# Kernel tuning notes

Measured on AMD Instinct MI355X. Metric: run time of the kernel, lower is better.

The kernel has to match this reference:

```python
import jax, jax.numpy as jnp
import numpy as np

N_NODES = 50000
N_EDGES = 800000
IN_DIM = 128
OUT_DIM = 64
REL_DIM = 32
NEG_SLOPE = 0.01  # torch F.leaky_relu default


def setup_inputs() -> dict:
    key = jax.random.key(0)
    k1, k2, k3, k4, k5, k6 = jax.random.split(key, 6)
    h = jax.random.normal(k1, (N_NODES, IN_DIM), dtype=jnp.float32)
    p = jax.random.normal(k2, (N_EDGES, REL_DIM), dtype=jnp.float32)
    src = jax.random.randint(k3, (N_EDGES,), 0, N_NODES, dtype=jnp.int32)
    dst = jax.random.randint(k4, (N_EDGES,), 0, N_NODES, dtype=jnp.int32)
    # torch Linear weights: [out_features, in_features], xavier-like scale
    W_fc = jax.random.normal(k5, (OUT_DIM, IN_DIM), dtype=jnp.float32) * (2.0 / (IN_DIM + OUT_DIM)) ** 0.5
    W_attn = jax.random.normal(k6, (1, 2 * OUT_DIM + REL_DIM), dtype=jnp.float32) * 0.1
    return {"h": h, "p": p, "src": src, "dst": dst, "W_fc": W_fc, "W_attn": W_attn}


def reference(h, p, src, dst, W_fc, W_attn):
    n = h.shape[0]
    z = h @ W_fc.T                       # [N, out_dim]
    z_src = z[src]                       # [E, out_dim] gather
    z_dst = z[dst]                       # [E, out_dim] gather
    feat = jnp.concatenate([z_src, p, z_dst], axis=1)  # [E, 2*out+rel]
    a = feat @ W_attn.T                  # [E, 1]
    e = jax.nn.leaky_relu(a[:, 0], NEG_SLOPE)          # [E]
    # segment softmax over incoming edges of each dst node
    seg_max = jax.ops.segment_max(e, dst, num_segments=n)  # [N]
    num = jnp.exp(e - seg_max[dst])                        # [E]
    denom = jax.ops.segment_sum(num, dst, num_segments=n)  # [N]
    alpha = num / denom[dst]                               # [E]
    # softmax-weighted message aggregation (scatter-add)
    h_out = jax.ops.segment_sum(alpha[:, None] * z_src, dst, num_segments=n)  # [N, out_dim]
    return h_out
```

## Files before the change

### kernel.cpp

```cpp
#include <hip/hip_runtime.h>
#include <hip/hip_bf16.h>

#define N_NODES 50000
#define N_EDGES 800000
#define IN_DIM 128
#define OUT_DIM 64
#define REL_DIM 32
#define NEG_SLOPE 0.01f
#define NB 391
#define K3_TILE 2048
#define K3_BLOCKS ((N_EDGES + K3_TILE - 1) / K3_TILE)
#define BWIN 2560
#define NBLK_A 782
#define K12_GRID 2346

__global__ __launch_bounds__(256) void k12_fused(const float* __restrict__ h,
                                                 const float* __restrict__ Wfc,
                                                 const float* __restrict__ Wattn,
                                                 const float* __restrict__ p,
                                                 __hip_bfloat16* __restrict__ zb,
                                                 float* __restrict__ s1,
                                                 float* __restrict__ s2,
                                                 float* __restrict__ dotp,
                                                 unsigned* __restrict__ ccur) {
    __shared__ float Wl[64][68];
    __shared__ float hl[64][68];
    const int t = threadIdx.x;
    const int b = blockIdx.x;

    if (b % 3 == 0) {
        const int blk = b / 3;
        const int cg = t & 15, ng = t >> 4;
        const int c0 = cg * 4;
        float wa1[4], wa2[4];
#pragma unroll
        for (int j = 0; j < 4; ++j) { wa1[j] = Wattn[c0 + j]; wa2[j] = Wattn[96 + c0 + j]; }

        const int n0 = blk * 64;
        float acc[4][4] = {};
        const float4* W4 = (const float4*)Wfc;
        const float4* h4 = (const float4*)h;

#pragma unroll
        for (int H = 0; H < 2; ++H) {
            __syncthreads();
#pragma unroll
            for (int i = 0; i < 4; ++i) {
                int idx = t + 256 * i;
                int c = idx & 63, k4 = idx >> 6;
                float4 v = W4[c * 32 + H * 16 + k4];
                Wl[4*k4+0][c] = v.x; Wl[4*k4+1][c] = v.y;
                Wl[4*k4+2][c] = v.z; Wl[4*k4+3][c] = v.w;
            }
#pragma unroll
            for (int i = 0; i < 4; ++i) {
                int idx = t + 256 * i;
                int n = idx & 63, k4 = idx >> 6;
                int gn = n0 + n; if (gn > N_NODES - 1) gn = N_NODES - 1;
                float4 v = h4[(size_t)gn * 32 + H * 16 + k4];
                hl[4*k4+0][n] = v.x; hl[4*k4+1][n] = v.y;
                hl[4*k4+2][n] = v.z; hl[4*k4+3][n] = v.w;
            }
            __syncthreads();
#pragma unroll 8
            for (int k = 0; k < 64; ++k) {
                float4 wv = *(const float4*)&Wl[k][c0];
                float4 hv = *(const float4*)&hl[k][ng * 4];
                float wvf[4] = {wv.x, wv.y, wv.z, wv.w};
                float hvf[4] = {hv.x, hv.y, hv.z, hv.w};
#pragma unroll
                for (int i = 0; i < 4; ++i)
#pragma unroll
                    for (int j = 0; j < 4; ++j) acc[i][j] += hvf[i] * wvf[j];
            }
        }

#pragma unroll
        for (int i = 0; i < 4; ++i) {
            int gn = n0 + ng * 4 + i;
            float r1 = acc[i][0]*wa1[0] + acc[i][1]*wa1[1] + acc[i][2]*wa1[2] + acc[i][3]*wa1[3];
            float r2 = acc[i][0]*wa2[0] + acc[i][1]*wa2[1] + acc[i][2]*wa2[2] + acc[i][3]*wa2[3];
#pragma unroll
            for (int off = 1; off < 16; off <<= 1) {
                r1 += __shfl_xor(r1, off, 64);
                r2 += __shfl_xor(r2, off, 64);
            }
            if (gn < N_NODES) {
                __hip_bfloat16 b0 = __float2bfloat16(acc[i][0]);
                __hip_bfloat16 b1 = __float2bfloat16(acc[i][1]);
                __hip_bfloat16 b2 = __float2bfloat16(acc[i][2]);
                __hip_bfloat16 b3 = __float2bfloat16(acc[i][3]);
                ushort4 st;
                st.x = *(unsigned short*)&b0; st.y = *(unsigned short*)&b1;
                st.z = *(unsigned short*)&b2; st.w = *(unsigned short*)&b3;
                ((ushort4*)zb)[(size_t)gn * 16 + cg] = st;
                if (cg == 0) { s1[gn] = r1; s2[gn] = r2; }
            }
        }
    } else {
        const int kb = b - b / 3 - 1;
        if (kb == 0) {
            for (int i = t; i < NB * 16; i += 256) ccur[i] = 0u;
        }
        const int tid = kb * 256 + t;
        if (tid < 400000) {
            const int q = tid & 7;
            const float w0 = Wattn[64 + q * 4 + 0];
            const float w1 = Wattn[64 + q * 4 + 1];
            const float w2 = Wattn[64 + q * 4 + 2];
            const float w3 = Wattn[64 + q * 4 + 3];
            const float4* p4 = (const float4*)p;
            const int a = tid >> 3;
#pragma unroll
            for (int half = 0; half < 2; ++half) {
                float4 v[8];
#pragma unroll
                for (int j = 0; j < 8; ++j) v[j] = p4[tid + (half * 8 + j) * 400000];
                float d[8];
#pragma unroll
                for (int j = 0; j < 8; ++j)
                    d[j] = v[j].x * w0 + v[j].y * w1 + v[j].z * w2 + v[j].w * w3;
#pragma unroll
                for (int off = 1; off < 8; off <<= 1)
#pragma unroll
                    for (int j = 0; j < 8; ++j) d[j] += __shfl_xor(d[j], off, 64);
                if (q == 0) {
#pragma unroll
                    for (int j = 0; j < 8; ++j)
                        dotp[a + (half * 8 + j) * 50000] = d[j];
                }
            }
        }
    }
}

__global__ __launch_bounds__(256) void k3_fused(const float* __restrict__ dotp,
                                                const int* __restrict__ src,
                                                const int* __restrict__ dst,
                                                const float* __restrict__ s1,
                                                const float* __restrict__ s2,
                                                unsigned* __restrict__ ccur,
                                                float2* __restrict__ pair) {
    __shared__ unsigned hist[NB];
    __shared__ unsigned gb[NB];
    __shared__ unsigned lcur[NB];
    const int t = threadIdx.x;
    for (int i = t; i < NB; i += 256) hist[i] = 0;
    __syncthreads();

    const int base = blockIdx.x * K3_TILE;
    float evr[8];
    unsigned auxr[8];
    short br[8];
#pragma unroll
    for (int i = 0; i < 8; ++i) {
        int e = base + i * 256 + t;
        if (e < N_EDGES) {
            int s = src[e], d = dst[e];
            float a = s1[s] + dotp[e] + s2[d];
            evr[i] = a > 0.f ? a : NEG_SLOPE * a;
            auxr[i] = (unsigned)s | ((unsigned)(d & 127) << 16);
            int bb = d >> 7;
            br[i] = (short)bb;
            atomicAdd(&hist[bb], 1u);
        } else br[i] = -1;
    }
    __syncthreads();
    for (int i = t; i < NB; i += 256) {
        lcur[i] = 0;
        gb[i] = hist[i] ? (i * BWIN + atomicAdd(&ccur[i * 16], hist[i])) : 0u;
    }
    __syncthreads();
#pragma unroll
    for (int i = 0; i < 8; ++i) {
        if (br[i] >= 0) {
            int bb = br[i];
            unsigned pos = atomicAdd(&lcur[bb], 1u);
            pair[gb[bb] + pos] = make_float2(evr[i], __uint_as_float(auxr[i]));
        }
    }
}

__global__ __launch_bounds__(256) void k3b_sort(const unsigned* __restrict__ ccur,
                                                const float2* __restrict__ pair,
                                                float2* __restrict__ pair2,
                                                unsigned* __restrict__ beg_g,
                                                unsigned* __restrict__ end_g) {
    __shared__ float2 items[BWIN];
    __shared__ unsigned hist[128], loffs[128], lcur[128], sd[128];
    const int t = threadIdx.x;
    const int b = blockIdx.x;
    const int base = b * BWIN;
    int cnt = (int)ccur[b * 16];
    if (cnt > BWIN) cnt = BWIN;
    if (t < 128) { hist[t] = 0; lcur[t] = 0; }
    __syncthreads();
    for (int i = t; i < cnt; i += 256) {
        float2 it = pair[base + i];
        items[i] = it;
        atomicAdd(&hist[__float_as_uint(it.y) >> 16], 1u);
    }
    __syncthreads();
    unsigned v = (t < 128) ? hist[t] : 0u;
    if (t < 128) sd[t] = v;
    __syncthreads();
#pragma unroll
    for (int off = 1; off < 128; off <<= 1) {
        unsigned tmp = (t >= off && t < 128) ? sd[t - off] : 0u;
        __syncthreads();
        if (t < 128) sd[t] += tmp;
        __syncthreads();
    }
    if (t < 128) {
        unsigned ex = sd[t] - v;
        loffs[t] = ex;
        beg_g[b * 128 + t] = base + ex;
        end_g[b * 128 + t] = base + ex + v;
    }
    __syncthreads();
    for (int i = t; i < cnt; i += 256) {
        float2 it = items[i];
        unsigned dl = __float_as_uint(it.y) >> 16;
        unsigned pos = atomicAdd(&lcur[dl], 1u);
        pair2[base + loffs[dl] + pos] = it;
    }
}

__global__ __launch_bounds__(256) void k4_agg(const unsigned* __restrict__ beg_g,
                                              const unsigned* __restrict__ end_g,
                                              const float2* __restrict__ pair2,
                                              const __hip_bfloat16* __restrict__ zb,
                                              float* __restrict__ out) {
    const int t = threadIdx.x;
    const int lane = t & 63;
    const int sub = lane >> 4;
    const int lc = lane & 15;
    const int wid = (blockIdx.x * 256 + t) >> 6;
    const int n = wid * 4 + sub;
    const int lo = beg_g[n], hi = end_g[n];
    const ushort* zs = (const ushort*)zb;
    float a0 = 0.f, a1 = 0.f, a2 = 0.f, a3 = 0.f, den = 0.f;
    int i = lo;
    for (; i + 3 < hi; i += 4) {
        float2 pr[4];
#pragma unroll
        for (int j = 0; j < 4; ++j) pr[j] = pair2[i + j];
        ushort4 zv[4];
#pragma unroll
        for (int j = 0; j < 4; ++j) {
            int s = __float_as_uint(pr[j].y) & 0xFFFF;
            zv[j] = *(const ushort4*)&zs[s * OUT_DIM + lc * 4];
        }
#pragma unroll
        for (int j = 0; j < 4; ++j) {
            float e = __expf(pr[j].x);
            a0 += e * __uint_as_float((unsigned)zv[j].x << 16);
            a1 += e * __uint_as_float((unsigned)zv[j].y << 16);
            a2 += e * __uint_as_float((unsigned)zv[j].z << 16);
            a3 += e * __uint_as_float((unsigned)zv[j].w << 16);
            den += e;
        }
    }
    for (; i < hi; ++i) {
        float2 p0 = pair2[i];
        int s = __float_as_uint(p0.y) & 0xFFFF;
        ushort4 zv = *(const ushort4*)&zs[s * OUT_DIM + lc * 4];
        float e = __expf(p0.x);
        a0 += e * __uint_as_float((unsigned)zv.x << 16);
        a1 += e * __uint_as_float((unsigned)zv.y << 16);
        a2 += e * __uint_as_float((unsigned)zv.z << 16);
        a3 += e * __uint_as_float((unsigned)zv.w << 16);
        den += e;
    }
    float4 st;
    if (hi > lo) {
        float inv = 1.f / den;
        st.x = a0 * inv; st.y = a1 * inv; st.z = a2 * inv; st.w = a3 * inv;
    } else {
        st.x = st.y = st.z = st.w = 0.f;
    }
    ((float4*)out)[(size_t)n * 16 + lc] = st;
}

extern "C" void kernel_launch(void* const* d_in, const int* in_sizes, int n_in,
                              void* d_out, int out_size, void* d_ws, size_t ws_size,
                              hipStream_t stream) {
    const float* h     = (const float*)d_in[0];
    const float* p     = (const float*)d_in[1];
    const int*   src   = (const int*)d_in[2];
    const int*   dst   = (const int*)d_in[3];
    const float* Wfc   = (const float*)d_in[4];
    const float* Wattn = (const float*)d_in[5];
    float* out = (float*)d_out;

    float* ws = (float*)d_ws;
    __hip_bfloat16* zb = (__hip_bfloat16*)ws;
    float*    s1     = ws + 1600000;
    float*    s2     = ws + 1650000;
    float*    dotp   = ws + 1700000;
    unsigned* ccur   = (unsigned*)(ws + 2500000);
    unsigned* beg_g  = (unsigned*)(ws + 2506272);
    unsigned* end_g  = (unsigned*)(ws + 2556320);
    float2*   pair   = (float2*)(ws + 2606368);
    float2*   pair2  = (float2*)(ws + 4608288);

    k12_fused<<<K12_GRID, 256, 0, stream>>>(h, Wfc, Wattn, p, zb, s1, s2, dotp, ccur);
    k3_fused<<<K3_BLOCKS, 256, 0, stream>>>(dotp, src, dst, s1, s2, ccur, pair);
    k3b_sort<<<NB, 256, 0, stream>>>(ccur, pair, pair2, beg_g, end_g);
    k4_agg<<<3125, 256, 0, stream>>>(beg_g, end_g, pair2, zb, out);
}
```

Baseline: 80.12 us.

## Shrink GEMM LDS tiles, raise occupancy hint, coalesce dotp stores via shuffles

The GEMM branch of the fused kernel now stages K in four 32-wide chunks instead of two 64-wide ones, halving shared memory per block, and declares a minimum of 8 blocks per SM through launch bounds to allow more resident blocks. The p-dot branch no longer has only one lane in eight write its eight results at strided addresses. Lanes now redistribute the reduced values with shuffles so every lane issues a single store, and the stores of a warp land on contiguous runs of addresses. The trade is twice as many syncthreads and tile loads per GEMM block, plus extra shuffle instructions and possible register pressure from the occupancy hint.

```diff
diff --git a/kernel.cpp b/kernel.cpp
--- a/kernel.cpp
+++ b/kernel.cpp
@@ -14,17 +14,17 @@
 #define NBLK_A 782
 #define K12_GRID 2346
 
-__global__ __launch_bounds__(256) void k12_fused(const float* __restrict__ h,
-                                                 const float* __restrict__ Wfc,
-                                                 const float* __restrict__ Wattn,
-                                                 const float* __restrict__ p,
-                                                 __hip_bfloat16* __restrict__ zb,
-                                                 float* __restrict__ s1,
-                                                 float* __restrict__ s2,
-                                                 float* __restrict__ dotp,
-                                                 unsigned* __restrict__ ccur) {
-    __shared__ float Wl[64][68];
-    __shared__ float hl[64][68];
+__global__ __launch_bounds__(256, 8) void k12_fused(const float* __restrict__ h,
+                                                    const float* __restrict__ Wfc,
+                                                    const float* __restrict__ Wattn,
+                                                    const float* __restrict__ p,
+                                                    __hip_bfloat16* __restrict__ zb,
+                                                    float* __restrict__ s1,
+                                                    float* __restrict__ s2,
+                                                    float* __restrict__ dotp,
+                                                    unsigned* __restrict__ ccur) {
+    __shared__ float Wl[32][68];
+    __shared__ float hl[32][68];
     const int t = threadIdx.x;
     const int b = blockIdx.x;
 
@@ -42,28 +42,28 @@
         const float4* h4 = (const float4*)h;
 
 #pragma unroll
-        for (int H = 0; H < 2; ++H) {
+        for (int Q = 0; Q < 4; ++Q) {
             __syncthreads();
 #pragma unroll
-            for (int i = 0; i < 4; ++i) {
+            for (int i = 0; i < 2; ++i) {
                 int idx = t + 256 * i;
-                int c = idx & 63, k4 = idx >> 6;
-                float4 v = W4[c * 32 + H * 16 + k4];
-                Wl[4*k4+0][c] = v.x; Wl[4*k4+1][c] = v.y;
-                Wl[4*k4+2][c] = v.z; Wl[4*k4+3][c] = v.w;
-            }
-#pragma unroll
-            for (int i = 0; i < 4; ++i) {
+                int c = idx & 63, k4l = idx >> 6;
+                float4 v = W4[c * 32 + Q * 8 + k4l];
+                Wl[4*k4l+0][c] = v.x; Wl[4*k4l+1][c] = v.y;
+                Wl[4*k4l+2][c] = v.z; Wl[4*k4l+3][c] = v.w;
+            }
+#pragma unroll
+            for (int i = 0; i < 2; ++i) {
                 int idx = t + 256 * i;
-                int n = idx & 63, k4 = idx >> 6;
+                int n = idx & 63, k4l = idx >> 6;
                 int gn = n0 + n; if (gn > N_NODES - 1) gn = N_NODES - 1;
-                float4 v = h4[(size_t)gn * 32 + H * 16 + k4];
-                hl[4*k4+0][n] = v.x; hl[4*k4+1][n] = v.y;
-                hl[4*k4+2][n] = v.z; hl[4*k4+3][n] = v.w;
+                float4 v = h4[(size_t)gn * 32 + Q * 8 + k4l];
+                hl[4*k4l+0][n] = v.x; hl[4*k4l+1][n] = v.y;
+                hl[4*k4l+2][n] = v.z; hl[4*k4l+3][n] = v.w;
             }
             __syncthreads();
 #pragma unroll 8
-            for (int k = 0; k < 64; ++k) {
+            for (int k = 0; k < 32; ++k) {
                 float4 wv = *(const float4*)&Wl[k][c0];
                 float4 hv = *(const float4*)&hl[k][ng * 4];
                 float wvf[4] = {wv.x, wv.y, wv.z, wv.w};
@@ -102,15 +102,16 @@
         if (kb == 0) {
             for (int i = t; i < NB * 16; i += 256) ccur[i] = 0u;
         }
+        const int lane = t & 63;
         const int tid = kb * 256 + t;
-        if (tid < 400000) {
+        const int a0 = (kb * 256 + (t & ~63)) >> 3;
+        if (a0 < 50000) {
             const int q = tid & 7;
             const float w0 = Wattn[64 + q * 4 + 0];
             const float w1 = Wattn[64 + q * 4 + 1];
             const float w2 = Wattn[64 + q * 4 + 2];
             const float w3 = Wattn[64 + q * 4 + 3];
             const float4* p4 = (const float4*)p;
-            const int a = tid >> 3;
 #pragma unroll
             for (int half = 0; half < 2; ++half) {
                 float4 v[8];
@@ -124,11 +125,13 @@
                 for (int off = 1; off < 8; off <<= 1)
 #pragma unroll
                     for (int j = 0; j < 8; ++j) d[j] += __shfl_xor(d[j], off, 64);
-                if (q == 0) {
-#pragma unroll
-                    for (int j = 0; j < 8; ++j)
-                        dotp[a + (half * 8 + j) * 50000] = d[j];
+                float val = 0.f;
+#pragma unroll
+                for (int j = 0; j < 8; ++j) {
+                    float tmp = __shfl(d[j], (lane & 7) * 8, 64);
+                    if ((lane >> 3) == j) val = tmp;
                 }
+                dotp[a0 + (lane & 7) + (half * 8 + (lane >> 3)) * 50000] = val;
             }
         }
     }
```

Result: no change. 81.11 us (+1.2%).
